# Kernel optimization log

Hardware: AMD Instinct MI355X
Metric: run time of the kernel (lower is better)

## Reference

```python
import jax, jax.numpy as jnp
import numpy as np

HIDDEN = 1024
LAYERS = 8
LETTERS = 100
INTER = 16


def setup_inputs() -> dict:
    key = jax.random.key(0)
    ks = jax.random.split(key, 12)
    s_i = 1.0 / np.sqrt(HIDDEN)
    website = jax.random.uniform(ks[0], (1, 2048, LETTERS), dtype=jnp.float32)
    payload = jax.random.uniform(ks[1], (1, 2048, LETTERS), dtype=jnp.float32)
    # stacked LSTMCell params: all cells take the raw input (input_size=LETTERS)
    W_ih = jax.random.uniform(ks[2], (LAYERS, 4 * HIDDEN, LETTERS), jnp.float32, -s_i, s_i)
    W_hh = jax.random.uniform(ks[3], (LAYERS, 4 * HIDDEN, HIDDEN), jnp.float32, -s_i, s_i)
    b_ih = jax.random.uniform(ks[4], (LAYERS, 4 * HIDDEN), jnp.float32, -s_i, s_i)
    b_hh = jax.random.uniform(ks[5], (LAYERS, 4 * HIDDEN), jnp.float32, -s_i, s_i)
    W_lin = jax.random.uniform(ks[6], (INTER, HIDDEN), jnp.float32, -s_i, s_i)
    b_lin = jax.random.uniform(ks[7], (INTER,), jnp.float32, -s_i, s_i)
    s_o = 1.0 / np.sqrt(INTER)
    W_out = jax.random.uniform(ks[8], (1, INTER), jnp.float32, -s_o, s_o)
    b_out = jax.random.uniform(ks[9], (1,), jnp.float32, -s_o, s_o)
    return {"website": website, "payload": payload, "W_ih": W_ih, "W_hh": W_hh,
            "b_ih": b_ih, "b_hh": b_hh, "W_lin": W_lin, "b_lin": b_lin,
            "W_out": W_out, "b_out": b_out}


def _lstm_cell(xt, h, c, Wi, Wh, bi, bh):
    # gates: [4H] = Wi @ xt + Wh @ h + biases (batch==1, stored as vectors)
    g = Wi @ xt + bi + Wh @ h + bh
    i, f, gg, o = jnp.split(g, 4)
    i = jax.nn.sigmoid(i)
    f = jax.nn.sigmoid(f)
    gg = jnp.tanh(gg)
    o = jax.nn.sigmoid(o)
    c2 = f * c + i * gg
    h2 = o * jnp.tanh(c2)
    return h2, c2


def _encoder(x, W_ih, W_hh, b_ih, b_hh, W_lin, b_lin):
    # x: [T, LETTERS] (batch 1 squeezed). One shared (h, c) threaded through
    # both the layer stack and time, exactly like the original code.
    H = W_hh.shape[-1]

    def step(carry, xt):
        def layer(carry, p):
            h, c = carry
            Wi, Wh, bi, bh = p
            return _lstm_cell(xt, h, c, Wi, Wh, bi, bh), None
        carry, _ = jax.lax.scan(layer, carry, (W_ih, W_hh, b_ih, b_hh))
        return carry, None

    init = (jnp.zeros((H,), x.dtype), jnp.zeros((H,), x.dtype))
    (h, c), _ = jax.lax.scan(step, init, x)
    # original applies the Linear to 'output' which is the CELL state c
    return W_lin @ c + b_lin  # [INTER]


def reference(website, payload, W_ih, W_hh, b_ih, b_hh, W_lin, b_lin, W_out, b_out):
    x = jnp.concatenate([website, payload], axis=1)[0]  # [T, LETTERS]
    feat = _encoder(x, W_ih, W_hh, b_ih, b_hh, W_lin, b_lin)  # [INTER]
    out = jax.nn.sigmoid(W_out @ feat + b_out)  # [1]
    return out.reshape(1, 1, 1)
```

## Files before the change

### kernel.cpp

```cpp
#include <hip/hip_runtime.h>
#include <stdint.h>

#define HID 1024
#define NLAYERS 8
#define NLET 100
#define T_TOTAL 4096

typedef uint32_t u32x4 __attribute__((ext_vector_type(4)));

__device__ __forceinline__ uint32_t f2bf(float f) {
    uint32_t u = __float_as_uint(f);
    return (u + 0x7FFFu + ((u >> 16) & 1u)) >> 16;
}
__device__ __forceinline__ float bflo(uint32_t p) { return __uint_as_float(p << 16); }
__device__ __forceinline__ float bfhi(uint32_t p) { return __uint_as_float(p & 0xFFFF0000u); }
__device__ __forceinline__ float sigm(float x) { return 1.0f / (1.0f + __expf(-x)); }
__device__ __forceinline__ float tanh_f(float x) {
    float xx = fminf(fmaxf(x, -15.0f), 15.0f);
    float e = __expf(2.0f * xx);
    return (e - 1.0f) / (e + 1.0f);
}
#define SBYTE(w, b) ((float)((int)((w) << (24 - 8 * (b))) >> 24))
__device__ __forceinline__ uint32_t rnd24(float f) {
    return (__float_as_uint(f) + 0x80u) >> 8;
}

__device__ __forceinline__ void store_coh_x4(void* p, u32x4 d) {
    asm volatile("global_store_dwordx4 %0, %1, off sc0 sc1" ::"v"(p), "v"(d) : "memory");
}
__device__ __forceinline__ void load_coh_x4(const void* p, u32x4& a) {
    asm volatile(
        "global_load_dwordx4 %0, %1, off sc0 sc1\n\t"
        "s_waitcnt vmcnt(0)"
        : "=v"(a)
        : "v"(p)
        : "memory");
}

__global__ void __launch_bounds__(256, 1)
lstm_persistent(const float* __restrict__ website, const float* __restrict__ payload,
                const float* __restrict__ W_ih, const float* __restrict__ W_hh,
                const float* __restrict__ b_ih, const float* __restrict__ b_hh,
                char* mail, float* c_out, int ncopies) {
    __shared__ float h_lds[HID];
    __shared__ float h_new[4];
    extern __shared__ __align__(16) uint8_t res_lds[];

    const int tid = threadIdx.x;
    const int b = blockIdx.x;
    const int u = tid >> 6;
    const int lane = tid & 63;
    const int k = b * 4 + u;
    const int rcopy = b & (ncopies - 1);

    uint32_t wh[NLAYERS][4][8];
    float wxf[NLAYERS][4][2];
    float bias[NLAYERS][4];
#pragma unroll
    for (int l = 0; l < NLAYERS; ++l) {
#pragma unroll
        for (int g = 0; g < 4; ++g) {
            const int row = 1024 * g + k;
            const float* src = W_hh + ((size_t)(l * 4096 + row)) * 1024;
            uint32_t rb[4];
#pragma unroll
            for (int p = 0; p < 8; ++p) {
                const int c0 = 2 * lane + 128 * p;
                const float w0 = src[c0], w1 = src[c0 + 1];
                const uint32_t pk = f2bf(w0) | (f2bf(w1) << 16);
                wh[l][g][p] = pk;
                const float r0 = (w0 - bflo(pk)) * 1048576.0f;
                const float r1 = (w1 - bfhi(pk)) * 1048576.0f;
                const int i0 = __float2int_rn(fminf(fmaxf(r0, -127.0f), 127.0f));
                const int i1 = __float2int_rn(fminf(fmaxf(r1, -127.0f), 127.0f));
                const uint32_t byt = ((uint32_t)i0 & 0xFFu) | (((uint32_t)i1 & 0xFFu) << 8);
                if ((p & 1) == 0) rb[p >> 1] = byt;
                else rb[p >> 1] |= (byt << 16);
            }
            {
                u32x4 v;
                v.x = rb[0]; v.y = rb[1]; v.z = rb[2]; v.w = rb[3];
                u32x4* dst = (u32x4*)res_lds + (((u * NLAYERS + l) * 4 + g) * 64 + lane);
                *dst = v;
            }
            if (lane < 50) {
                const float* sx = W_ih + ((size_t)(l * 4096 + row)) * NLET + 2 * lane;
                wxf[l][g][0] = sx[0];
                wxf[l][g][1] = sx[1];
            } else {
                wxf[l][g][0] = 0.f;
                wxf[l][g][1] = 0.f;
            }
            bias[l][g] = b_ih[l * 4096 + row] + b_hh[l * 4096 + row];
        }
    }

    ((float4*)h_lds)[tid] = make_float4(0.f, 0.f, 0.f, 0.f);
    float c = 0.0f;
    int dl = 6;
    __syncthreads();

    for (int t = 0; t < T_TOTAL; ++t) {
        float x0 = 0.f, x1 = 0.f;
        if (lane < 50) {
            const float* xp = (t < 2048) ? (website + (size_t)t * NLET)
                                         : (payload + (size_t)(t - 2048) * NLET);
            x0 = xp[2 * lane];
            x1 = xp[2 * lane + 1];
        }
#pragma unroll
        for (int l = 0; l < NLAYERS; ++l) {
            const int s = t * NLAYERS + l + 1;
            const int par = s & 1;

            float2 hv[8];
#pragma unroll
            for (int p = 0; p < 8; ++p)
                hv[p] = *(const float2*)&h_lds[2 * lane + 128 * p];
            const u32x4* rr = (const u32x4*)res_lds + ((u * NLAYERS + l) * 4) * 64 + lane;
            const u32x4 rg0 = rr[0];
            const u32x4 rg1 = rr[64];
            const u32x4 rg2 = rr[128];
            const u32x4 rg3 = rr[192];

            float acc0 = 0.f, acc1 = 0.f, acc2 = 0.f, acc3 = 0.f;
#pragma unroll
            for (int p = 0; p < 8; ++p) {
                const float hA = hv[p].x, hB = hv[p].y;
                uint32_t w;
                w = wh[l][0][p]; acc0 = fmaf(bflo(w), hA, acc0); acc0 = fmaf(bfhi(w), hB, acc0);
                w = wh[l][1][p]; acc1 = fmaf(bflo(w), hA, acc1); acc1 = fmaf(bfhi(w), hB, acc1);
                w = wh[l][2][p]; acc2 = fmaf(bflo(w), hA, acc2); acc2 = fmaf(bfhi(w), hB, acc2);
                w = wh[l][3][p]; acc3 = fmaf(bflo(w), hA, acc3); acc3 = fmaf(bfhi(w), hB, acc3);
            }
            float ra0 = 0.f, ra1 = 0.f, ra2 = 0.f, ra3 = 0.f;
#pragma unroll
            for (int p = 0; p < 8; ++p) {
                const float hA = hv[p].x, hB = hv[p].y;
                const int b0 = 2 * (p & 1), b1 = 2 * (p & 1) + 1;
                uint32_t w;
                w = rg0[p >> 1]; ra0 = fmaf(SBYTE(w, b0), hA, ra0); ra0 = fmaf(SBYTE(w, b1), hB, ra0);
                w = rg1[p >> 1]; ra1 = fmaf(SBYTE(w, b0), hA, ra1); ra1 = fmaf(SBYTE(w, b1), hB, ra1);
                w = rg2[p >> 1]; ra2 = fmaf(SBYTE(w, b0), hA, ra2); ra2 = fmaf(SBYTE(w, b1), hB, ra2);
                w = rg3[p >> 1]; ra3 = fmaf(SBYTE(w, b0), hA, ra3); ra3 = fmaf(SBYTE(w, b1), hB, ra3);
            }
            acc0 = fmaf(ra0, 0x1.0p-20f, acc0);
            acc1 = fmaf(ra1, 0x1.0p-20f, acc1);
            acc2 = fmaf(ra2, 0x1.0p-20f, acc2);
            acc3 = fmaf(ra3, 0x1.0p-20f, acc3);
            acc0 = fmaf(wxf[l][0][0], x0, acc0); acc0 = fmaf(wxf[l][0][1], x1, acc0);
            acc1 = fmaf(wxf[l][1][0], x0, acc1); acc1 = fmaf(wxf[l][1][1], x1, acc1);
            acc2 = fmaf(wxf[l][2][0], x0, acc2); acc2 = fmaf(wxf[l][2][1], x1, acc2);
            acc3 = fmaf(wxf[l][3][0], x0, acc3); acc3 = fmaf(wxf[l][3][1], x1, acc3);

#pragma unroll
            for (int mm = 32; mm > 0; mm >>= 1) {
                acc0 += __shfl_xor(acc0, mm, 64);
                acc1 += __shfl_xor(acc1, mm, 64);
                acc2 += __shfl_xor(acc2, mm, 64);
                acc3 += __shfl_xor(acc3, mm, 64);
            }
            const float gi = sigm(acc0 + bias[l][0]);
            const float gf = sigm(acc1 + bias[l][1]);
            const float gg = tanh_f(acc2 + bias[l][2]);
            const float go = sigm(acc3 + bias[l][3]);
            c = fmaf(gf, c, gi * gg);
            const float hn = go * tanh_f(c);
            if (lane == 0) h_new[u] = hn;
            __syncthreads();

            if (tid < ncopies) {
                const uint32_t t0 = rnd24(h_new[0]);
                const uint32_t t1 = rnd24(h_new[1]);
                const uint32_t t2 = rnd24(h_new[2]);
                const uint32_t t3 = rnd24(h_new[3]);
                u32x4 d;
                d.x = (t0 << 8) | (t1 >> 16);
                d.y = (t1 << 16) | (t2 >> 8);
                d.z = (t2 << 24) | t3;
                d.w = (uint32_t)s;
                char* dst = mail + ((size_t)((tid * 2 + par) * 256 + b)) * 16;
                store_coh_x4(dst, d);
            }

            {
                const char* srcp = mail + ((size_t)((rcopy * 2 + par) * 256 + tid)) * 16;
                for (int i = 0; i < dl; ++i) __builtin_amdgcn_s_sleep(8);
                u32x4 a;
                int retries = 0;
                for (;;) {
                    load_coh_x4(srcp, a);
                    if (a.w == (uint32_t)s) break;
                    ++retries;
                    __builtin_amdgcn_s_sleep(8);
                }
                dl = (retries == 0) ? (dl > 0 ? dl - 1 : 0)
                                    : ((dl + retries > 48) ? 48 : dl + retries);
                h_lds[4 * tid + 0] = __uint_as_float(a.x & 0xFFFFFF00u);
                h_lds[4 * tid + 1] = __uint_as_float(((a.x & 0xFFu) << 24) | ((a.y >> 16) << 8));
                h_lds[4 * tid + 2] = __uint_as_float(((a.y & 0xFFFFu) << 16) | ((a.z >> 24) << 8));
                h_lds[4 * tid + 3] = __uint_as_float((a.z & 0xFFFFFFu) << 8);
            }
            __syncthreads();
        }
    }

    if (lane == 0) c_out[k] = c;
}

__global__ void head_kernel(const float* __restrict__ c_out, const float* __restrict__ W_lin,
                            const float* __restrict__ b_lin, const float* __restrict__ W_out,
                            const float* __restrict__ b_out, float* out) {
    const int lane = threadIdx.x;
    float cv[16];
    const float4* cp = (const float4*)(c_out + lane * 16);
#pragma unroll
    for (int q = 0; q < 4; ++q) {
        float4 v = cp[q];
        cv[4 * q + 0] = v.x;
        cv[4 * q + 1] = v.y;
        cv[4 * q + 2] = v.z;
        cv[4 * q + 3] = v.w;
    }
    float fsum = 0.f;
#pragma unroll
    for (int i = 0; i < 16; ++i) {
        const float* w = W_lin + (size_t)i * HID + lane * 16;
        float a = 0.f;
#pragma unroll
        for (int m = 0; m < 16; ++m) a = fmaf(w[m], cv[m], a);
#pragma unroll
        for (int mm = 32; mm > 0; mm >>= 1) a += __shfl_xor(a, mm, 64);
        fsum = fmaf(W_out[i], a + b_lin[i], fsum);
    }
    if (lane == 0) out[0] = sigm(fsum + b_out[0]);
}

extern "C" void kernel_launch(void* const* d_in, const int* in_sizes, int n_in, void* d_out,
                              int out_size, void* d_ws, size_t ws_size, hipStream_t stream) {
    (void)in_sizes; (void)n_in; (void)out_size;
    const float* website = (const float*)d_in[0];
    const float* payload = (const float*)d_in[1];
    const float* W_ih = (const float*)d_in[2];
    const float* W_hh = (const float*)d_in[3];
    const float* b_ih = (const float*)d_in[4];
    const float* b_hh = (const float*)d_in[5];
    const float* W_lin = (const float*)d_in[6];
    const float* b_lin = (const float*)d_in[7];
    const float* W_out = (const float*)d_in[8];
    const float* b_out = (const float*)d_in[9];

    int ncopies = 64;
    while (ncopies > 1 && (size_t)ncopies * 8192 + 4096 > ws_size) ncopies >>= 1;
    char* mail = (char*)d_ws;
    float* c_out = (float*)((char*)d_ws + (size_t)ncopies * 8192);

    hipMemsetAsync(mail, 0, (size_t)ncopies * 8192, stream);
    lstm_persistent<<<256, 256, 131072, stream>>>(website, payload, W_ih, W_hh, b_ih, b_hh,
                                                  mail, c_out, ncopies);
    head_kernel<<<1, 64, 0, stream>>>(c_out, W_lin, b_lin, W_out, b_out, (float*)d_out);
}
```

Baseline: 283.5 ms.

## Use per-XCC relay blocks to fan out hidden state via local L2

Replaces the 64-copy system-coherent mailbox broadcast with one central mailbox. One elected relay block per XCC polls it and republishes the full hidden vector into an XCC-local buffer using L2-scope stores. The other blocks then poll their local L2 copy, falling back to the coherent central copy after many retries. This cuts cross-die coherent traffic per step, but it adds an extra hop of latency through the relay and relies on blocks sharing an XCC also sharing an L2.

```diff
diff --git a/kernel.cpp b/kernel.cpp
--- a/kernel.cpp
+++ b/kernel.cpp
@@ -32,18 +32,36 @@
     asm volatile(
         "global_load_dwordx4 %0, %1, off sc0 sc1\n\t"
         "s_waitcnt vmcnt(0)"
-        : "=v"(a)
-        : "v"(p)
-        : "memory");
+        : "=v"(a) : "v"(p) : "memory");
+}
+__device__ __forceinline__ void load_coh_64(const void* p, u32x4& a, u32x4& b, u32x4& c,
+                                            u32x4& d) {
+    asm volatile(
+        "global_load_dwordx4 %0, %4, off sc0 sc1\n\t"
+        "global_load_dwordx4 %1, %4, off offset:16 sc0 sc1\n\t"
+        "global_load_dwordx4 %2, %4, off offset:32 sc0 sc1\n\t"
+        "global_load_dwordx4 %3, %4, off offset:48 sc0 sc1\n\t"
+        "s_waitcnt vmcnt(0)"
+        : "=v"(a), "=v"(b), "=v"(c), "=v"(d) : "v"(p) : "memory");
+}
+__device__ __forceinline__ void store_l2_x4(void* p, u32x4 d) {
+    asm volatile("global_store_dwordx4 %0, %1, off sc0" ::"v"(p), "v"(d) : "memory");
+}
+__device__ __forceinline__ void load_l2_x4(const void* p, u32x4& a) {
+    asm volatile(
+        "global_load_dwordx4 %0, %1, off sc0\n\t"
+        "s_waitcnt vmcnt(0)"
+        : "=v"(a) : "v"(p) : "memory");
 }
 
 __global__ void __launch_bounds__(256, 1)
 lstm_persistent(const float* __restrict__ website, const float* __restrict__ payload,
                 const float* __restrict__ W_ih, const float* __restrict__ W_hh,
                 const float* __restrict__ b_ih, const float* __restrict__ b_hh,
-                char* mail, float* c_out, int ncopies) {
+                char* central, char* localb, int* counters, float* c_out) {
     __shared__ float h_lds[HID];
     __shared__ float h_new[4];
+    __shared__ int s_xcc, s_relay;
     extern __shared__ __align__(16) uint8_t res_lds[];
 
     const int tid = threadIdx.x;
@@ -51,7 +69,6 @@
     const int u = tid >> 6;
     const int lane = tid & 63;
     const int k = b * 4 + u;
-    const int rcopy = b & (ncopies - 1);
 
     uint32_t wh[NLAYERS][4][8];
     float wxf[NLAYERS][4][2];
@@ -95,10 +112,18 @@
         }
     }
 
+    if (tid == 0) {
+        int xcc = __builtin_amdgcn_s_getreg(20 | (0 << 6) | (31 << 11)) & 7;
+        s_xcc = xcc;
+        s_relay = (atomicAdd(&counters[xcc], 1) == 0) ? 1 : 0;
+    }
+
     ((float4*)h_lds)[tid] = make_float4(0.f, 0.f, 0.f, 0.f);
     float c = 0.0f;
     int dl = 6;
     __syncthreads();
+    const int myxcc = s_xcc;
+    const int relay = s_relay;
 
     for (int t = 0; t < T_TOTAL; ++t) {
         float x0 = 0.f, x1 = 0.f;
@@ -169,7 +194,7 @@
             if (lane == 0) h_new[u] = hn;
             __syncthreads();
 
-            if (tid < ncopies) {
+            if (tid == 0) {
                 const uint32_t t0 = rnd24(h_new[0]);
                 const uint32_t t1 = rnd24(h_new[1]);
                 const uint32_t t2 = rnd24(h_new[2]);
@@ -179,23 +204,44 @@
                 d.y = (t1 << 16) | (t2 >> 8);
                 d.z = (t2 << 24) | t3;
                 d.w = (uint32_t)s;
-                char* dst = mail + ((size_t)((tid * 2 + par) * 256 + b)) * 16;
-                store_coh_x4(dst, d);
-            }
-
-            {
-                const char* srcp = mail + ((size_t)((rcopy * 2 + par) * 256 + tid)) * 16;
+                store_coh_x4(central + ((size_t)(par * 256 + b)) * 16, d);
+            }
+
+            if (relay && tid < 64) {
+                const char* cen = central + ((size_t)(par * 256 + 4 * lane)) * 16;
                 for (int i = 0; i < dl; ++i) __builtin_amdgcn_s_sleep(8);
-                u32x4 a;
+                u32x4 a0, a1, a2, a3;
                 int retries = 0;
                 for (;;) {
-                    load_coh_x4(srcp, a);
-                    if (a.w == (uint32_t)s) break;
+                    load_coh_64(cen, a0, a1, a2, a3);
+                    if (a0.w == (uint32_t)s && a1.w == (uint32_t)s &&
+                        a2.w == (uint32_t)s && a3.w == (uint32_t)s)
+                        break;
                     ++retries;
                     __builtin_amdgcn_s_sleep(8);
                 }
                 dl = (retries == 0) ? (dl > 0 ? dl - 1 : 0)
                                     : ((dl + retries > 48) ? 48 : dl + retries);
+                char* loc = localb + ((size_t)((myxcc * 2 + par) * 256 + 4 * lane)) * 16;
+                store_l2_x4(loc, a0);
+                store_l2_x4(loc + 16, a1);
+                store_l2_x4(loc + 32, a2);
+                store_l2_x4(loc + 48, a3);
+            }
+
+            {
+                const char* lp =
+                    localb + ((size_t)((myxcc * 2 + par) * 256 + tid)) * 16;
+                const char* cp = central + ((size_t)(par * 256 + tid)) * 16;
+                u32x4 a;
+                int r = 0;
+                for (;;) {
+                    if (r < 128) load_l2_x4(lp, a);
+                    else         load_coh_x4(cp, a);
+                    if (a.w == (uint32_t)s) break;
+                    ++r;
+                    __builtin_amdgcn_s_sleep(2);
+                }
                 h_lds[4 * tid + 0] = __uint_as_float(a.x & 0xFFFFFF00u);
                 h_lds[4 * tid + 1] = __uint_as_float(((a.x & 0xFFu) << 24) | ((a.y >> 16) << 8));
                 h_lds[4 * tid + 2] = __uint_as_float(((a.y & 0xFFFFu) << 16) | ((a.z >> 24) << 8));
@@ -238,7 +284,7 @@
 
 extern "C" void kernel_launch(void* const* d_in, const int* in_sizes, int n_in, void* d_out,
                               int out_size, void* d_ws, size_t ws_size, hipStream_t stream) {
-    (void)in_sizes; (void)n_in; (void)out_size;
+    (void)in_sizes; (void)n_in; (void)out_size; (void)ws_size;
     const float* website = (const float*)d_in[0];
     const float* payload = (const float*)d_in[1];
     const float* W_ih = (const float*)d_in[2];
@@ -250,13 +296,13 @@
     const float* W_out = (const float*)d_in[8];
     const float* b_out = (const float*)d_in[9];
 
-    int ncopies = 64;
-    while (ncopies > 1 && (size_t)ncopies * 8192 + 4096 > ws_size) ncopies >>= 1;
-    char* mail = (char*)d_ws;
-    float* c_out = (float*)((char*)d_ws + (size_t)ncopies * 8192);
-
-    hipMemsetAsync(mail, 0, (size_t)ncopies * 8192, stream);
+    char* central = (char*)d_ws;
+    char* localb = (char*)d_ws + 8192;
+    int* counters = (int*)((char*)d_ws + 73728);
+    float* c_out = (float*)((char*)d_ws + 73984);
+
+    hipMemsetAsync(d_ws, 0, 73760, stream);
     lstm_persistent<<<256, 256, 131072, stream>>>(website, payload, W_ih, W_hh, b_ih, b_hh,
-                                                  mail, c_out, ncopies);
+                                                  central, localb, counters, c_out);
     head_kernel<<<1, 64, 0, stream>>>(c_out, W_lin, b_lin, W_out, b_out, (float*)d_out);
 }
```

Result: slower. 916.1 ms (+223.1%).
